# Optimization experiments

Hardware: AMD Instinct MI355X
Metric: run time of the kernel (lower is better)

Reference implementation:

```python
import jax, jax.numpy as jnp
import numpy as np

N_KNOTS = 16
D_LATENT = 32
DEGREE = 3
GRID = (256, 256, 256)


def _de_boor(x, t, c, degree):
    """Vectorized de Boor B-spline evaluation.
    x: [...] query points; t: [n_knots+6] padded knots; c: [n_knots+2] control points."""
    k = jnp.digitize(x, t) - 1  # [...] int32 segment index per query point
    d = [c[j + k - degree] for j in range(degree + 1)]  # degree+1 gathers, each shaped like x
    for r in range(1, degree + 1):
        for j in range(degree, r - 1, -1):
            t_lo = t[j + k - degree]
            t_hi = t[j + 1 + k - r]
            alpha = (x - t_lo) / (t_hi - t_lo)
            d[j] = (1.0 - alpha) * d[j - 1] + alpha * d[j]
    return d[degree]


def setup_inputs() -> dict:
    key = jax.random.key(0)
    ks = jax.random.split(key, 6)
    d, n = D_LATENT, N_KNOTS
    s = lambda m: 1.0 / np.sqrt(m)
    return {
        "x": jax.random.uniform(ks[0], GRID, jnp.float32, 0.0, 1.7),  # |k| grid, fftfreq-normalized
        "a": jax.random.uniform(ks[1], (1,), jnp.float32, 0.1, 1.0),  # scale factor
        "W1": jax.random.normal(ks[2], (1, d), jnp.float32),
        "b1": jnp.zeros((d,), jnp.float32),
        "W2": jax.random.normal(ks[3], (d, d), jnp.float32) * s(d),
        "b2": jnp.zeros((d,), jnp.float32),
        "Ww": jax.random.normal(ks[4], (d, n + 1), jnp.float32) * s(d),
        "bw": jnp.zeros((n + 1,), jnp.float32),
        "Wk": jax.random.normal(ks[5], (d, n - 1), jnp.float32) * s(d),
        "bk": jnp.zeros((n - 1,), jnp.float32),
    }


def reference(x, a, W1, b1, W2, b2, Ww, bw, Wk, bk):
    # tiny sin-MLP on the scalar scale factor a
    net = jnp.sin(a @ W1 + b1)          # [d_latent]
    net = jnp.sin(net @ W2 + b2)        # [d_latent]
    w = net @ Ww + bw                   # [n_knots+1] control-point deltas
    k = net @ Wk + bk                   # [n_knots-1] knot logits
    # monotone knot positions in (0,1], prepend 0
    k = jnp.concatenate([jnp.zeros((1,), x.dtype), jnp.cumsum(jax.nn.softmax(k))])
    w = jnp.concatenate([jnp.zeros((1,), x.dtype), w])  # [n_knots+2] control points
    # pad knots for degree-3 spline: 3 zeros, internal knots, 3 ones
    ak = jnp.concatenate([jnp.zeros((3,), x.dtype), k, jnp.ones((3,), x.dtype)])
    xc = jnp.clip(x / jnp.sqrt(jnp.asarray(3.0, x.dtype)), 0.0, 1.0 - 1e-4)
    return _de_boor(xc, ak, w, DEGREE)
```

## Files before the change

### kernel.cpp

```cpp
#include <hip/hip_runtime.h>
#include <math.h>


__device__ __forceinline__ float deboor_eval(float x, int k, const float* t, const float* c) {
    float d[4];
#pragma unroll
    for (int j = 0; j < 4; ++j) d[j] = c[j + k - 3];
#pragma unroll
    for (int r = 1; r <= 3; ++r) {
#pragma unroll
        for (int j = 3; j >= 1; --j) {
            if (j < r) continue;
            float tlo = t[j + k - 3];
            float thi = t[j + 1 + k - r];
            float al = (x - tlo) / (thi - tlo);
            d[j] = (1.0f - al) * d[j - 1] + al * d[j];
        }
    }
    return d[3];
}

__global__ void spline_setup_kernel(
    const float* __restrict__ a,  const float* __restrict__ W1, const float* __restrict__ b1,
    const float* __restrict__ W2, const float* __restrict__ b2,
    const float* __restrict__ Ww, const float* __restrict__ bw,
    const float* __restrict__ Wk, const float* __restrict__ bk,
    float* __restrict__ ws)
{
    __shared__ float net1[32], net2[32], cpt[18], kl[15], ak[22];
    int t = threadIdx.x;
    float av = a[0];

    if (t < 32) net1[t] = sinf(av * W1[t] + b1[t]);
    __syncthreads();

    if (t < 32) {
        float s = b2[t];
#pragma unroll
        for (int i = 0; i < 32; ++i) s += net1[i] * W2[i * 32 + t];
        net2[t] = sinf(s);
    }
    __syncthreads();

    if (t < 17) {
        float s = bw[t];
#pragma unroll
        for (int i = 0; i < 32; ++i) s += net2[i] * Ww[i * 17 + t];
        cpt[t + 1] = s;
    }
    if (t == 63) cpt[0] = 0.0f;
    if (t >= 32 && t < 47) {
        int j = t - 32;
        float s = bk[j];
#pragma unroll
        for (int i = 0; i < 32; ++i) s += net2[i] * Wk[i * 15 + j];
        kl[j] = s;
    }
    __syncthreads();

    if (t == 0) {
        float m = kl[0];
        for (int j = 1; j < 15; ++j) m = fmaxf(m, kl[j]);
        float e[15], sum = 0.0f;
        for (int j = 0; j < 15; ++j) { e[j] = expf(kl[j] - m); sum += e[j]; }
        float inv = 1.0f / sum;
        ak[0] = ak[1] = ak[2] = 0.0f;
        ak[3] = 0.0f;
        float cum = 0.0f;
        for (int j = 0; j < 15; ++j) { cum += e[j]; ak[4 + j] = cum * inv; }
        ak[19] = ak[20] = ak[21] = 1.0f;
    }
    __syncthreads();

    if (t < 14) ws[t] = ak[4 + t];

    if (t < 15) {
        int k = t + 3;
        float t0 = ak[k], t1 = ak[k + 1];
        float dl = (t1 - t0) * (1.0f / 3.0f);
        float f0 = deboor_eval(t0,              k, ak, cpt);
        float f1 = deboor_eval(t0 + dl,         k, ak, cpt);
        float f2 = deboor_eval(t0 + 2.0f * dl,  k, ak, cpt);
        float f3 = deboor_eval(t0 + 3.0f * dl,  k, ak, cpt);
        float idl  = 1.0f / dl;
        float g01  = (f1 - f0) * idl, g12 = (f2 - f1) * idl, g23 = (f3 - f2) * idl;
        float h012 = (g12 - g01) * (0.5f * idl), h123 = (g23 - g12) * (0.5f * idl);
        float q    = (h123 - h012) * (idl * (1.0f / 3.0f));
        float c0 = f0;
        float c1 = g01 - dl * h012 + 2.0f * dl * dl * q;
        float c2 = h012 - 3.0f * dl * q;
        float c3 = q;
        ws[16 + t] = t0;
        ws[32 + t] = c0;
        ws[48 + t] = c1;
        ws[64 + t] = c2;
        ws[80 + t] = c3;
    }
}

__global__ __launch_bounds__(256) void spline_eval_kernel(
    const float* __restrict__ x, const float* __restrict__ p,
    float* __restrict__ out, int n)
{
    __shared__ float sStart[15], sC0[15], sC1[15], sC2[15], sC3[15];
    int t = threadIdx.x;
    if (t < 15) {
        sStart[t] = p[16 + t];
        sC0[t]    = p[32 + t];
        sC1[t]    = p[48 + t];
        sC2[t]    = p[64 + t];
        sC3[t]    = p[80 + t];
    }
    float bb[14];
#pragma unroll
    for (int j = 0; j < 14; ++j) bb[j] = p[j];
    __syncthreads();

    const float kInvSqrt3 = 0.57735026918962576f;
    const float kXMax     = 1.0f - 1e-4f;

    int n4 = n >> 2;
    int gtid = blockIdx.x * blockDim.x + t;
    int stride = gridDim.x * blockDim.x;
    const float4* x4 = (const float4*)x;
    float4* o4 = (float4*)out;

    for (int i = gtid; i < n4; i += stride) {
        float4 xv = x4[i];
        float vv[4] = {xv.x, xv.y, xv.z, xv.w};
        float rr[4];
#pragma unroll
        for (int e = 0; e < 4; ++e) {
            float xc = fminf(fmaxf(vv[e] * kInvSqrt3, 0.0f), kXMax);
            int s = 0;
#pragma unroll
            for (int j = 0; j < 14; ++j) s += (xc >= bb[j]) ? 1 : 0;
            float u = xc - sStart[s];
            rr[e] = fmaf(fmaf(fmaf(sC3[s], u, sC2[s]), u, sC1[s]), u, sC0[s]);
        }
        float4 r; r.x = rr[0]; r.y = rr[1]; r.z = rr[2]; r.w = rr[3];
        o4[i] = r;
    }
    for (int i = (n4 << 2) + gtid; i < n; i += stride) {
        float xc = fminf(fmaxf(x[i] * kInvSqrt3, 0.0f), kXMax);
        int s = 0;
#pragma unroll
        for (int j = 0; j < 14; ++j) s += (xc >= bb[j]) ? 1 : 0;
        float u = xc - sStart[s];
        out[i] = fmaf(fmaf(fmaf(sC3[s], u, sC2[s]), u, sC1[s]), u, sC0[s]);
    }
}

extern "C" void kernel_launch(void* const* d_in, const int* in_sizes, int n_in,
                              void* d_out, int out_size, void* d_ws, size_t ws_size,
                              hipStream_t stream)
{
    const float* x  = (const float*)d_in[0];
    const float* a  = (const float*)d_in[1];
    const float* W1 = (const float*)d_in[2];
    const float* b1 = (const float*)d_in[3];
    const float* W2 = (const float*)d_in[4];
    const float* b2 = (const float*)d_in[5];
    const float* Ww = (const float*)d_in[6];
    const float* bw = (const float*)d_in[7];
    const float* Wk = (const float*)d_in[8];
    const float* bk = (const float*)d_in[9];
    float* ws  = (float*)d_ws;
    float* out = (float*)d_out;

    spline_setup_kernel<<<1, 64, 0, stream>>>(a, W1, b1, W2, b2, Ww, bw, Wk, bk, ws);
    spline_eval_kernel<<<2048, 256, 0, stream>>>(x, ws, out, out_size);
}
```

Before: 135.3 us.

## Fuse spline setup into eval kernel, recomputing coefficients per block

Merges the single-block setup kernel into the streaming eval kernel, so each of the 2048 blocks recomputes the small MLP, softmax knots and per-segment cubic coefficients into shared memory. This removes one kernel launch and the dependency gap between the two kernels, as well as the workspace round trip. In exchange every block does redundant serial setup work, including a single-thread softmax and several barriers, before it starts streaming x.

```diff
diff --git a/kernel.cpp b/kernel.cpp
--- a/kernel.cpp
+++ b/kernel.cpp
@@ -20,18 +20,19 @@
     return d[3];
 }
 
-__global__ void spline_setup_kernel(
+__global__ __launch_bounds__(256) void spline_fused_kernel(
+    const float* __restrict__ x,
     const float* __restrict__ a,  const float* __restrict__ W1, const float* __restrict__ b1,
     const float* __restrict__ W2, const float* __restrict__ b2,
     const float* __restrict__ Ww, const float* __restrict__ bw,
     const float* __restrict__ Wk, const float* __restrict__ bk,
-    float* __restrict__ ws)
+    float* __restrict__ out, int n)
 {
     __shared__ float net1[32], net2[32], cpt[18], kl[15], ak[22];
+    __shared__ float sB[14], sStart[15], sC0[15], sC1[15], sC2[15], sC3[15];
     int t = threadIdx.x;
-    float av = a[0];
 
-    if (t < 32) net1[t] = sinf(av * W1[t] + b1[t]);
+    if (t < 32) net1[t] = sinf(a[0] * W1[t] + b1[t]);
     __syncthreads();
 
     if (t < 32) {
@@ -61,18 +62,17 @@
     if (t == 0) {
         float m = kl[0];
         for (int j = 1; j < 15; ++j) m = fmaxf(m, kl[j]);
-        float e[15], sum = 0.0f;
-        for (int j = 0; j < 15; ++j) { e[j] = expf(kl[j] - m); sum += e[j]; }
+        float sum = 0.0f;
+        for (int j = 0; j < 15; ++j) { float e = expf(kl[j] - m); ak[4 + j] = e; sum += e; }
         float inv = 1.0f / sum;
-        ak[0] = ak[1] = ak[2] = 0.0f;
-        ak[3] = 0.0f;
+        ak[0] = ak[1] = ak[2] = ak[3] = 0.0f;
         float cum = 0.0f;
-        for (int j = 0; j < 15; ++j) { cum += e[j]; ak[4 + j] = cum * inv; }
+        for (int j = 0; j < 15; ++j) { cum += ak[4 + j]; ak[4 + j] = cum * inv; }
         ak[19] = ak[20] = ak[21] = 1.0f;
     }
     __syncthreads();
 
-    if (t < 14) ws[t] = ak[4 + t];
+    if (t < 14) sB[t] = ak[4 + t];
 
     if (t < 15) {
         int k = t + 3;
@@ -86,35 +86,17 @@
         float g01  = (f1 - f0) * idl, g12 = (f2 - f1) * idl, g23 = (f3 - f2) * idl;
         float h012 = (g12 - g01) * (0.5f * idl), h123 = (g23 - g12) * (0.5f * idl);
         float q    = (h123 - h012) * (idl * (1.0f / 3.0f));
-        float c0 = f0;
-        float c1 = g01 - dl * h012 + 2.0f * dl * dl * q;
-        float c2 = h012 - 3.0f * dl * q;
-        float c3 = q;
-        ws[16 + t] = t0;
-        ws[32 + t] = c0;
-        ws[48 + t] = c1;
-        ws[64 + t] = c2;
-        ws[80 + t] = c3;
+        sStart[t] = t0;
+        sC0[t]    = f0;
+        sC1[t]    = g01 - dl * h012 + 2.0f * dl * dl * q;
+        sC2[t]    = h012 - 3.0f * dl * q;
+        sC3[t]    = q;
     }
-}
+    __syncthreads();
 
-__global__ __launch_bounds__(256) void spline_eval_kernel(
-    const float* __restrict__ x, const float* __restrict__ p,
-    float* __restrict__ out, int n)
-{
-    __shared__ float sStart[15], sC0[15], sC1[15], sC2[15], sC3[15];
-    int t = threadIdx.x;
-    if (t < 15) {
-        sStart[t] = p[16 + t];
-        sC0[t]    = p[32 + t];
-        sC1[t]    = p[48 + t];
-        sC2[t]    = p[64 + t];
-        sC3[t]    = p[80 + t];
-    }
     float bb[14];
 #pragma unroll
-    for (int j = 0; j < 14; ++j) bb[j] = p[j];
-    __syncthreads();
+    for (int j = 0; j < 14; ++j) bb[j] = sB[j];
 
     const float kInvSqrt3 = 0.57735026918962576f;
     const float kXMax     = 1.0f - 1e-4f;
@@ -165,9 +147,9 @@
     const float* bw = (const float*)d_in[7];
     const float* Wk = (const float*)d_in[8];
     const float* bk = (const float*)d_in[9];
-    float* ws  = (float*)d_ws;
     float* out = (float*)d_out;
 
-    spline_setup_kernel<<<1, 64, 0, stream>>>(a, W1, b1, W2, b2, Ww, bw, Wk, bk, ws);
-    spline_eval_kernel<<<2048, 256, 0, stream>>>(x, ws, out, out_size);
+    (void)d_ws; (void)ws_size;
+    spline_fused_kernel<<<2048, 256, 0, stream>>>(x, a, W1, b1, W2, b2, Ww, bw, Wk, bk,
+                                                  out, out_size);
 }
```

After: 133.3 us. About the same (-1.4%).
